# Performance work log

Measured on AMD Instinct MI355X. Metric: run time of the kernel, lower is better.

The kernel has to match this reference:

```python
import jax, jax.numpy as jnp
import numpy as np

N_NODES = 100_000
N_EDGES = 1_600_000
N_GRAPHS = 512
D_NODE = 128
H = 128
L_EXTRA = 2  # model_layer - 1


def _bn(x, g, b, eps=1e-5):
    # BatchNorm1d, training-mode math (biased batch variance), eval dropout = identity
    mu = jnp.mean(x, axis=0)
    var = jnp.var(x, axis=0)
    return g * (x - mu) * jax.lax.rsqrt(var + eps) + b


def _gin_conv(x, src, dst, W1, b1, bng, bnb, W2, b2):
    # GINConv (eps=0): mlp(x + sum_{j->i} x_j); mlp = Lin -> BN -> ReLU -> Lin
    agg = jax.ops.segment_sum(x[src], dst, num_segments=x.shape[0])
    h = x + agg
    h = jax.nn.relu(_bn(h @ W1 + b1, bng, bnb))
    return h @ W2 + b2


def setup_inputs():
    key = jax.random.key(0)
    ks = jax.random.split(key, 24)
    s = 0.05
    d = {}
    d["x"] = jax.random.normal(ks[0], (N_NODES, D_NODE), dtype=jnp.float32)
    d["edge_index"] = jax.random.randint(ks[1], (2, N_EDGES), 0, N_NODES, dtype=jnp.int32)
    d["batch"] = jnp.sort(jax.random.randint(ks[2], (N_NODES,), 0, N_GRAPHS, dtype=jnp.int32))
    d["vn_emb"] = jax.random.normal(ks[3], (1, H)) * s
    # conv1 MLP: Linear(D_NODE, 2H) -> BN -> ReLU -> Linear(2H, H)
    d["c1_W1"] = jax.random.normal(ks[4], (D_NODE, 2 * H)) * s
    d["c1_b1"] = jnp.zeros((2 * H,))
    d["c1_bng"] = jnp.ones((2 * H,))
    d["c1_bnb"] = jnp.zeros((2 * H,))
    d["c1_W2"] = jax.random.normal(ks[5], (2 * H, H)) * s
    d["c1_b2"] = jnp.zeros((H,))
    d["bn1_g"] = jnp.ones((H,))
    d["bn1_b"] = jnp.zeros((H,))
    # stacked extra GIN layers (model_layer - 1)
    d["cW1"] = jax.random.normal(ks[6], (L_EXTRA, H, 2 * H)) * s
    d["cb1"] = jnp.zeros((L_EXTRA, 2 * H))
    d["cbng"] = jnp.ones((L_EXTRA, 2 * H))
    d["cbnb"] = jnp.zeros((L_EXTRA, 2 * H))
    d["cW2"] = jax.random.normal(ks[7], (L_EXTRA, 2 * H, H)) * s
    d["cb2"] = jnp.zeros((L_EXTRA, H))
    d["bns_g"] = jnp.ones((L_EXTRA, H))
    d["bns_b"] = jnp.zeros((L_EXTRA, H))
    # virtual node MLP: Lin(H,2H)->BN->ReLU->Lin(2H,H)->BN->ReLU->Dropout
    d["vW1"] = jax.random.normal(ks[8], (H, 2 * H)) * s
    d["vb1"] = jnp.zeros((2 * H,))
    d["vbn1_g"] = jnp.ones((2 * H,))
    d["vbn1_b"] = jnp.zeros((2 * H,))
    d["vW2"] = jax.random.normal(ks[9], (2 * H, H)) * s
    d["vb2"] = jnp.zeros((H,))
    d["vbn2_g"] = jnp.ones((H,))
    d["vbn2_b"] = jnp.zeros((H,))
    return d


def reference(x, edge_index, batch, vn_emb, c1_W1, c1_b1, c1_bng, c1_bnb, c1_W2, c1_b2,
              bn1_g, bn1_b, cW1, cb1, cbng, cbnb, cW2, cb2, bns_g, bns_b,
              vW1, vb1, vbn1_g, vbn1_b, vW2, vb2, vbn2_g, vbn2_b):
    src, dst = edge_index[0], edge_index[1]
    # virtual node feature per graph: Embedding(1, H) indexed with zeros
    vfeat = jnp.broadcast_to(vn_emb[0], (N_GRAPHS, H))
    # layer 1: dropout is identity in eval mode
    post = jax.nn.relu(_bn(_gin_conv(x, src, dst, c1_W1, c1_b1, c1_bng, c1_bnb, c1_W2, c1_b2), bn1_g, bn1_b))
    for i in range(L_EXTRA):
        post = post + vfeat[batch]                       # virtual-node broadcast
        post = _bn(_gin_conv(post, src, dst, cW1[i], cb1[i], cbng[i], cbnb[i], cW2[i], cb2[i]), bns_g[i], bns_b[i])
        if i < L_EXTRA - 1:
            post = jax.nn.relu(post)
            pooled = jax.ops.segment_sum(post, batch, num_segments=N_GRAPHS)  # GlobalAddPool
            z = pooled + vfeat
            z = jax.nn.relu(_bn(z @ vW1 + vb1, vbn1_g, vbn1_b))
            vfeat = jax.nn.relu(_bn(z @ vW2 + vb2, vbn2_g, vbn2_b))
    # readout: global mean pool over nodes per graph
    counts = jax.ops.segment_sum(jnp.ones((x.shape[0],), post.dtype), batch, num_segments=N_GRAPHS)
    out = jax.ops.segment_sum(post, batch, num_segments=N_GRAPHS) / jnp.maximum(counts, 1.0)[:, None]
    return out
```

## Files before the change

kernel.cpp:

```cpp
#include <hip/hip_runtime.h>

#define NN 100000
#define NE 1600000
#define NG 512
#define DH 128
#define DH2 256
#define SCB 98
#define NSTRIPE 32

typedef __attribute__((ext_vector_type(8))) _Float16 h8;
typedef __attribute__((ext_vector_type(2))) _Float16 h2;
typedef __attribute__((ext_vector_type(4))) float f4;

static inline size_t align256(size_t x) { return (x + 255) & ~size_t(255); }

__global__ __launch_bounds__(256) void countslot_k(const int* __restrict__ ei,
                                                   int* __restrict__ cursor,
                                                   int* __restrict__ slot) {
    int i = blockIdx.x * blockDim.x + threadIdx.x;
    int stride = gridDim.x * blockDim.x;
    for (int e = i; e < NE; e += stride)
        slot[e] = atomicAdd(&cursor[ei[NE + e]], 1);
}

__global__ __launch_bounds__(256) void place_k(const int* __restrict__ ei,
                                               const int* __restrict__ rowptr,
                                               const int* __restrict__ slot,
                                               int* __restrict__ esrc) {
    int i = blockIdx.x * blockDim.x + threadIdx.x;
    int stride = gridDim.x * blockDim.x;
    for (int e = i; e < NE; e += stride)
        esrc[rowptr[ei[NE + e]] + slot[e]] = ei[e];
}

__global__ void gbound_k(const int* __restrict__ batch, int* __restrict__ gcnt) {
    int g = blockIdx.x * blockDim.x + threadIdx.x;
    if (g >= NG) return;
    int lo = 0, hi = NN;
    while (lo < hi) { int m = (lo + hi) >> 1; if (batch[m] < g) lo = m + 1; else hi = m; }
    int b0 = lo;
    lo = 0; hi = NN;
    int g1 = g + 1;
    while (lo < hi) { int m = (lo + hi) >> 1; if (batch[m] < g1) lo = m + 1; else hi = m; }
    gcnt[g] = lo - b0;
}

__global__ __launch_bounds__(256) void scan1_k(const int* __restrict__ deg,
                                               int* __restrict__ part) {
    int i0 = blockIdx.x * 1024 + threadIdx.x * 4;
    int s = 0;
    if (i0 < NN) {
        int4 v = *(const int4*)(deg + i0);
        s = v.x + v.y + v.z + v.w;
    }
#pragma unroll
    for (int o = 1; o < 64; o <<= 1) s += __shfl_xor(s, o);
    __shared__ int ws[4];
    if ((threadIdx.x & 63) == 0) ws[threadIdx.x >> 6] = s;
    __syncthreads();
    if (threadIdx.x == 0) part[blockIdx.x] = ws[0] + ws[1] + ws[2] + ws[3];
}

__global__ void scan2_k(int* __restrict__ part, int* __restrict__ rowptr) {
    if (threadIdx.x == 0) {
        int run = 0;
        for (int i = 0; i < SCB; i++) { int v = part[i]; part[i] = run; run += v; }
        rowptr[NN] = run;
    }
}

__global__ __launch_bounds__(256) void scan3_k(const int* __restrict__ deg,
                                               const int* __restrict__ part,
                                               int* __restrict__ rowptr) {
    int t = threadIdx.x;
    int i0 = blockIdx.x * 1024 + t * 4;
    int4 v = {0, 0, 0, 0};
    if (i0 < NN) v = *(const int4*)(deg + i0);
    int s = v.x + v.y + v.z + v.w;
    __shared__ int sc[256];
    sc[t] = s;
    __syncthreads();
    for (int o = 1; o < 256; o <<= 1) {
        int add = (t >= o) ? sc[t - o] : 0;
        __syncthreads();
        sc[t] += add;
        __syncthreads();
    }
    int excl = (t ? sc[t - 1] : 0) + part[blockIdx.x];
    if (i0 < NN) {
        int4 r;
        r.x = excl;
        r.y = excl + v.x;
        r.z = excl + v.x + v.y;
        r.w = excl + v.x + v.y + v.z;
        *(int4*)(rowptr + i0) = r;
    }
}

__global__ void castx_k(const float* __restrict__ x, _Float16* __restrict__ xh) {
    int i = blockIdx.x * blockDim.x + threadIdx.x;
    if (i >= NN * 16) return;
    const float4* s = (const float4*)x + i * 2;
    float4 p = s[0], q = s[1];
    h8 h = {(_Float16)p.x, (_Float16)p.y, (_Float16)p.z, (_Float16)p.w,
            (_Float16)q.x, (_Float16)q.y, (_Float16)q.z, (_Float16)q.w};
    ((h8*)xh)[i] = h;
}

__global__ void vinit_k(const float* __restrict__ emb, _Float16* __restrict__ vfeat) {
    int i = blockIdx.x * blockDim.x + threadIdx.x;
    if (i < NG * DH) vfeat[i] = (_Float16)emb[i & (DH - 1)];
}

__global__ void zin_k(const float* __restrict__ pooled, const _Float16* __restrict__ vf,
                      _Float16* __restrict__ zb) {
    int i = blockIdx.x * blockDim.x + threadIdx.x;
    if (i < NG * DH) zb[i] = (_Float16)(pooled[i] + (float)vf[i]);
}

__global__ void addvn_k(_Float16* __restrict__ x, const _Float16* __restrict__ vfeat,
                        const int* __restrict__ batch) {
    int i = blockIdx.x * blockDim.x + threadIdx.x;
    if (i >= NN * 16) return;
    int row = i >> 4;
    int bg = batch[row];
    h8 u = ((h8*)x)[i];
    h8 v = ((const h8*)vfeat)[bg * 16 + (i & 15)];
    h8 o;
#pragma unroll
    for (int e = 0; e < 8; e++) o[e] = (_Float16)((float)u[e] + (float)v[e]);
    ((h8*)x)[i] = o;
}

__global__ void finalout_k(const float* __restrict__ pooled2, const int* __restrict__ gcnt,
                           float* __restrict__ outp) {
    int i = blockIdx.x * blockDim.x + threadIdx.x;
    if (i >= NG * DH) return;
    float cnt = (float)gcnt[i >> 7];
    outp[i] = pooled2[i] / fmaxf(cnt, 1.0f);
}

__global__ void bnfin_k(const float* __restrict__ csum, const float* __restrict__ csq,
                        const float* __restrict__ g, const float* __restrict__ b,
                        float* __restrict__ scale, float* __restrict__ shift,
                        int NC, int M) {
    int col = threadIdx.x;
    if (col >= NC) return;
    float s = 0.f, q = 0.f;
    for (int st = 0; st < NSTRIPE; st++) { s += csum[st * NC + col]; q += csq[st * NC + col]; }
    float invM = 1.0f / (float)M;
    float mean = s * invM;
    float var = q * invM - mean * mean;
    float sc = g[col] * rsqrtf(var + 1e-5f);
    scale[col] = sc;
    shift[col] = b[col] - mean * sc;
}

struct WPack {
    const float* w[8];
    _Float16* wt[8];
    int K[8];
    int N[8];
};
__global__ void wtrans_k(WPack p) {
    int id = blockIdx.z;
    const float* W = p.w[id];
    _Float16* Wt = p.wt[id];
    int K = p.K[id], N = p.N[id];
    int n0 = blockIdx.x * 32, k0 = blockIdx.y * 32;
    if (n0 >= N || k0 >= K) return;
    __shared__ float t[32][33];
    int tx = threadIdx.x & 31, ty = threadIdx.x >> 5;
    for (int i = 0; i < 32; i += 8)
        t[ty + i][tx] = W[(size_t)(k0 + ty + i) * N + n0 + tx];
    __syncthreads();
    for (int i = 0; i < 32; i += 8)
        Wt[(size_t)(n0 + ty + i) * K + k0 + tx] = (_Float16)t[tx][ty + i];
}

__global__ __launch_bounds__(256) void agg_k(const _Float16* __restrict__ xin,
                                             const int* __restrict__ rowptr,
                                             const int* __restrict__ esrc,
                                             _Float16* __restrict__ out) {
    int wave = threadIdx.x >> 6, lane = threadIdx.x & 63;
    int node = blockIdx.x * 4 + wave;
    if (node >= NN) return;
    const h2* xr = (const h2*)xin;
    h2 self = xr[(size_t)node * 64 + lane];
    float a0 = (float)self.x, a1 = (float)self.y;
    int beg = rowptr[node], end = rowptr[node + 1];
    int j = beg;
    for (; j + 7 < end; j += 8) {
        int s0 = esrc[j],     s1 = esrc[j + 1], s2 = esrc[j + 2], s3 = esrc[j + 3];
        int s4 = esrc[j + 4], s5 = esrc[j + 5], s6 = esrc[j + 6], s7 = esrc[j + 7];
        h2 u0 = xr[(size_t)s0 * 64 + lane];
        h2 u1 = xr[(size_t)s1 * 64 + lane];
        h2 u2 = xr[(size_t)s2 * 64 + lane];
        h2 u3 = xr[(size_t)s3 * 64 + lane];
        h2 u4 = xr[(size_t)s4 * 64 + lane];
        h2 u5 = xr[(size_t)s5 * 64 + lane];
        h2 u6 = xr[(size_t)s6 * 64 + lane];
        h2 u7 = xr[(size_t)s7 * 64 + lane];
        a0 += ((float)u0.x + (float)u1.x) + ((float)u2.x + (float)u3.x)
            + ((float)u4.x + (float)u5.x) + ((float)u6.x + (float)u7.x);
        a1 += ((float)u0.y + (float)u1.y) + ((float)u2.y + (float)u3.y)
            + ((float)u4.y + (float)u5.y) + ((float)u6.y + (float)u7.y);
    }
    for (; j < end; j++) {
        h2 u = xr[(size_t)esrc[j] * 64 + lane];
        a0 += (float)u.x; a1 += (float)u.y;
    }
    h2 o; o.x = (_Float16)a0; o.y = (_Float16)a1;
    ((h2*)out)[(size_t)node * 64 + lane] = o;
}

__global__ __launch_bounds__(256, 2) void gemmA_k(
        const _Float16* __restrict__ A, const _Float16* __restrict__ Wt,
        const float* __restrict__ bias, _Float16* __restrict__ C,
        float* __restrict__ csum, float* __restrict__ csq, int M) {
    constexpr int K = 128, NCF = 256;
    constexpr int LDA = K + 8;
    __shared__ __align__(16) _Float16 As[128 * LDA];
    const int tid = threadIdx.x;
    const int lane = tid & 63;
    const int wave = tid >> 6;
    const int wr = wave & 1, wc = wave >> 1;
    const int lm = lane & 15, lq = lane >> 4;
    const int mB = blockIdx.x * 128;

    const int sr = tid >> 4;
    const int sc = (tid & 15) * 8;
#pragma unroll
    for (int rr = 0; rr < 128; rr += 16) {
        int gr = mB + rr + sr; if (gr >= M) gr = M - 1;
        *(h8*)&As[(rr + sr) * LDA + sc] = *(const h8*)&A[(size_t)gr * K + sc];
    }
    __syncthreads();

    f4 acc[4][8];
#pragma unroll
    for (int i = 0; i < 4; i++)
#pragma unroll
        for (int jj = 0; jj < 8; jj++) acc[i][jj] = (f4){0.f, 0.f, 0.f, 0.f};
#pragma unroll
    for (int ct = 0; ct < 2; ct++) {
        const int n0 = ct * 128 + wc * 64;
#pragma unroll
        for (int ks = 0; ks < 4; ks++) {
            h8 af[4], bf[4];
#pragma unroll
            for (int t = 0; t < 4; t++) {
                af[t] = *(const h8*)&As[(wr * 64 + t * 16 + lm) * LDA + ks * 32 + lq * 8];
                bf[t] = *(const h8*)&Wt[(size_t)(n0 + t * 16 + lm) * K + ks * 32 + lq * 8];
            }
#pragma unroll
            for (int i = 0; i < 4; i++)
#pragma unroll
                for (int j = 0; j < 4; j++)
                    acc[i][ct * 4 + j] =
                        __builtin_amdgcn_mfma_f32_16x16x32_f16(af[i], bf[j], acc[i][ct * 4 + j], 0, 0, 0);
        }
    }

    float bv[8];
#pragma unroll
    for (int jj = 0; jj < 8; jj++) bv[jj] = bias[(jj >> 2) * 128 + wc * 64 + (jj & 3) * 16 + lm];
    float ls[8] = {0, 0, 0, 0, 0, 0, 0, 0}, lsq[8] = {0, 0, 0, 0, 0, 0, 0, 0};
    _Float16* Cs = As;
    const int trow = tid >> 4;
    const int tcol = (tid & 15) * 8;
#pragma unroll
    for (int half = 0; half < 2; half++) {
        __syncthreads();
#pragma unroll
        for (int i = 0; i < 4; i++) {
            int row = wr * 64 + i * 16 + lq * 4;
#pragma unroll
            for (int j = 0; j < 4; j++) {
                int jj = half * 4 + j;
#pragma unroll
                for (int r = 0; r < 4; r++) {
                    float v = acc[i][jj][r] + bv[jj];
                    Cs[(row + r) * LDA + wc * 64 + j * 16 + lm] = (_Float16)v;
                    if (mB + row + r < M) { ls[jj] += v; lsq[jj] += v * v; }
                }
            }
        }
        __syncthreads();
#pragma unroll
        for (int p = 0; p < 8; p++) {
            int row = p * 16 + trow;
            int grow = mB + row;
            if (grow < M) {
                h8 v = *(const h8*)&Cs[row * LDA + tcol];
                *(h8*)&C[(size_t)grow * NCF + half * 128 + tcol] = v;
            }
        }
    }
    const int stripe = blockIdx.x & (NSTRIPE - 1);
#pragma unroll
    for (int jj = 0; jj < 8; jj++) {
        float s = ls[jj], q = lsq[jj];
        s += __shfl_xor(s, 16); s += __shfl_xor(s, 32);
        q += __shfl_xor(q, 16); q += __shfl_xor(q, 32);
        if (lq == 0) {
            int col = (jj >> 2) * 128 + wc * 64 + (jj & 3) * 16 + lm;
            atomicAdd(&csum[stripe * NCF + col], s);
            atomicAdd(&csq[stripe * NCF + col], q);
        }
    }
}

__global__ __launch_bounds__(256, 2) void gemmB_k(
        const _Float16* __restrict__ A, const _Float16* __restrict__ Wt,
        const float* __restrict__ bias, _Float16* __restrict__ C,
        float* __restrict__ csum, float* __restrict__ csq, int M,
        const float* __restrict__ bnsc, const float* __restrict__ bnsh) {
    constexpr int K = 256, NCF = 128, BK = 128;
    constexpr int LDA = BK + 8;
    __shared__ __align__(16) _Float16 As[128 * LDA];
    const int tid = threadIdx.x;
    const int lane = tid & 63;
    const int wave = tid >> 6;
    const int wr = wave & 1, wc = wave >> 1;
    const int lm = lane & 15, lq = lane >> 4;
    const int mB = blockIdx.x * 128;
    const int n0 = wc * 64;

    f4 acc[4][4];
#pragma unroll
    for (int i = 0; i < 4; i++)
#pragma unroll
        for (int j = 0; j < 4; j++) acc[i][j] = (f4){0.f, 0.f, 0.f, 0.f};

    const int sr = tid >> 4;
    const int sc = (tid & 15) * 8;

    for (int kc = 0; kc < K; kc += BK) {
        if (kc) __syncthreads();
        float bscv[8], bshv[8];
        {
            float4 s0 = *(const float4*)&bnsc[kc + sc];
            float4 s1 = *(const float4*)&bnsc[kc + sc + 4];
            float4 t0 = *(const float4*)&bnsh[kc + sc];
            float4 t1 = *(const float4*)&bnsh[kc + sc + 4];
            bscv[0] = s0.x; bscv[1] = s0.y; bscv[2] = s0.z; bscv[3] = s0.w;
            bscv[4] = s1.x; bscv[5] = s1.y; bscv[6] = s1.z; bscv[7] = s1.w;
            bshv[0] = t0.x; bshv[1] = t0.y; bshv[2] = t0.z; bshv[3] = t0.w;
            bshv[4] = t1.x; bshv[5] = t1.y; bshv[6] = t1.z; bshv[7] = t1.w;
        }
#pragma unroll
        for (int rr = 0; rr < 128; rr += 16) {
            int gr = mB + rr + sr; if (gr >= M) gr = M - 1;
            h8 h = *(const h8*)&A[(size_t)gr * K + kc + sc];
#pragma unroll
            for (int e = 0; e < 8; e++)
                h[e] = (_Float16)fmaxf((float)h[e] * bscv[e] + bshv[e], 0.f);
            *(h8*)&As[(rr + sr) * LDA + sc] = h;
        }
        __syncthreads();
#pragma unroll
        for (int ks = 0; ks < BK / 32; ks++) {
            h8 af[4], bf[4];
#pragma unroll
            for (int t = 0; t < 4; t++) {
                af[t] = *(const h8*)&As[(wr * 64 + t * 16 + lm) * LDA + ks * 32 + lq * 8];
                bf[t] = *(const h8*)&Wt[(size_t)(n0 + t * 16 + lm) * K + kc + ks * 32 + lq * 8];
            }
#pragma unroll
            for (int i = 0; i < 4; i++)
#pragma unroll
                for (int j = 0; j < 4; j++)
                    acc[i][j] = __builtin_amdgcn_mfma_f32_16x16x32_f16(af[i], bf[j], acc[i][j], 0, 0, 0);
        }
    }

    float bv[4];
#pragma unroll
    for (int j = 0; j < 4; j++) bv[j] = bias[n0 + j * 16 + lm];
    float ls[4] = {0, 0, 0, 0}, lsq[4] = {0, 0, 0, 0};
    __syncthreads();
    _Float16* Cs = As;
#pragma unroll
    for (int i = 0; i < 4; i++) {
        int row = wr * 64 + i * 16 + lq * 4;
        bool rv[4];
#pragma unroll
        for (int r = 0; r < 4; r++) rv[r] = (mB + row + r) < M;
#pragma unroll
        for (int j = 0; j < 4; j++) {
#pragma unroll
            for (int r = 0; r < 4; r++) {
                float v = acc[i][j][r] + bv[j];
                Cs[(row + r) * LDA + wc * 64 + j * 16 + lm] = (_Float16)v;
                if (rv[r]) { ls[j] += v; lsq[j] += v * v; }
            }
        }
    }
    const int stripe = blockIdx.x & (NSTRIPE - 1);
#pragma unroll
    for (int j = 0; j < 4; j++) {
        float s = ls[j], q = lsq[j];
        s += __shfl_xor(s, 16); s += __shfl_xor(s, 32);
        q += __shfl_xor(q, 16); q += __shfl_xor(q, 32);
        if (lq == 0) {
            atomicAdd(&csum[stripe * NCF + n0 + j * 16 + lm], s);
            atomicAdd(&csq[stripe * NCF + n0 + j * 16 + lm], q);
        }
    }
    __syncthreads();
    const int trow = tid >> 4;
    const int tcol = (tid & 15) * 8;
#pragma unroll
    for (int p = 0; p < 8; p++) {
        int row = p * 16 + trow;
        int grow = mB + row;
        if (grow < M) {
            h8 v = *(const h8*)&Cs[row * LDA + tcol];
            *(h8*)&C[(size_t)grow * NCF + tcol] = v;
        }
    }
}

__global__ void bnrelu_k(const _Float16* __restrict__ in, _Float16* __restrict__ out,
                         const float* __restrict__ scale, const float* __restrict__ shift,
                         const _Float16* __restrict__ vfeat, const int* __restrict__ batch,
                         int M) {
    constexpr int PER = 16;
    int tid = blockIdx.x * blockDim.x + threadIdx.x;
    int c8 = tid % PER;
    int c0 = c8 * 8;
    float sc[8], sh[8];
    float4 s0 = *(const float4*)&scale[c0];
    float4 s1 = *(const float4*)&scale[c0 + 4];
    float4 t0 = *(const float4*)&shift[c0];
    float4 t1 = *(const float4*)&shift[c0 + 4];
    sc[0] = s0.x; sc[1] = s0.y; sc[2] = s0.z; sc[3] = s0.w;
    sc[4] = s1.x; sc[5] = s1.y; sc[6] = s1.z; sc[7] = s1.w;
    sh[0] = t0.x; sh[1] = t0.y; sh[2] = t0.z; sh[3] = t0.w;
    sh[4] = t1.x; sh[5] = t1.y; sh[6] = t1.z; sh[7] = t1.w;
    int total = M * PER;
    int stride = gridDim.x * blockDim.x;
    for (int i = tid; i < total; i += stride) {
        int row = i / PER;
        h8 u = ((const h8*)in)[i];
        h8 w;
        bool vn = (vfeat != nullptr);
        if (vn) w = ((const h8*)vfeat)[batch[row] * PER + c8];
        h8 o;
#pragma unroll
        for (int e = 0; e < 8; e++) {
            float vv = fmaxf((float)u[e] * sc[e] + sh[e], 0.f);
            if (vn) vv += (float)w[e];
            o[e] = (_Float16)vv;
        }
        ((h8*)out)[i] = o;
    }
}

__global__ __launch_bounds__(256) void bnpool_k(
        const _Float16* __restrict__ in, _Float16* __restrict__ out,
        const float* __restrict__ scale, const float* __restrict__ shift,
        const int* __restrict__ batch, float* __restrict__ pooled,
        int M, int relu) {
    int t = threadIdx.x;
    int c0 = (t & 63) * 2;
    int r0 = blockIdx.x * 128 + (t >> 6) * 32;
    float sc0 = scale[c0], h0 = shift[c0];
    float sc1 = scale[c0 + 1], h1 = shift[c0 + 1];
    int rend = r0 + 32; if (rend > M) rend = M;
    float a0 = 0.f, a1 = 0.f; int cur = -1;
    int r = r0;
    for (; r + 1 < rend; r += 2) {
        h2 ua = ((const h2*)in)[(size_t)r * 64 + (c0 >> 1)];
        h2 ub = ((const h2*)in)[(size_t)(r + 1) * 64 + (c0 >> 1)];
        int bga = batch[r], bgb = batch[r + 1];
        float va0 = (float)ua.x * sc0 + h0, va1 = (float)ua.y * sc1 + h1;
        float vb0 = (float)ub.x * sc0 + h0, vb1 = (float)ub.y * sc1 + h1;
        if (relu) {
            va0 = fmaxf(va0, 0.f); va1 = fmaxf(va1, 0.f);
            vb0 = fmaxf(vb0, 0.f); vb1 = fmaxf(vb1, 0.f);
        }
        if (out) {
            h2 oa; oa.x = (_Float16)va0; oa.y = (_Float16)va1;
            h2 ob; ob.x = (_Float16)vb0; ob.y = (_Float16)vb1;
            ((h2*)out)[(size_t)r * 64 + (c0 >> 1)] = oa;
            ((h2*)out)[(size_t)(r + 1) * 64 + (c0 >> 1)] = ob;
        }
        if (bga != cur) {
            if (cur >= 0) {
                atomicAdd(&pooled[(size_t)cur * DH + c0], a0);
                atomicAdd(&pooled[(size_t)cur * DH + c0 + 1], a1);
            }
            cur = bga; a0 = 0.f; a1 = 0.f;
        }
        a0 += va0; a1 += va1;
        if (bgb != cur) {
            atomicAdd(&pooled[(size_t)cur * DH + c0], a0);
            atomicAdd(&pooled[(size_t)cur * DH + c0 + 1], a1);
            cur = bgb; a0 = 0.f; a1 = 0.f;
        }
        a0 += vb0; a1 += vb1;
    }
    for (; r < rend; r++) {
        h2 u = ((const h2*)in)[(size_t)r * 64 + (c0 >> 1)];
        float v0 = (float)u.x * sc0 + h0;
        float v1 = (float)u.y * sc1 + h1;
        if (relu) { v0 = fmaxf(v0, 0.f); v1 = fmaxf(v1, 0.f); }
        if (out) { h2 o; o.x = (_Float16)v0; o.y = (_Float16)v1; ((h2*)out)[(size_t)r * 64 + (c0 >> 1)] = o; }
        int bg = batch[r];
        if (bg != cur) {
            if (cur >= 0) {
                atomicAdd(&pooled[(size_t)cur * DH + c0], a0);
                atomicAdd(&pooled[(size_t)cur * DH + c0 + 1], a1);
            }
            cur = bg; a0 = 0.f; a1 = 0.f;
        }
        a0 += v0; a1 += v1;
    }
    if (cur >= 0) {
        atomicAdd(&pooled[(size_t)cur * DH + c0], a0);
        atomicAdd(&pooled[(size_t)cur * DH + c0 + 1], a1);
    }
}

extern "C" void kernel_launch(void* const* d_in, const int* in_sizes, int n_in,
                              void* d_out, int out_size, void* d_ws, size_t ws_size,
                              hipStream_t stream) {
    const float* x      = (const float*)d_in[0];
    const int*   ei     = (const int*)d_in[1];
    const int*   batch  = (const int*)d_in[2];
    const float* vn_emb = (const float*)d_in[3];
    const float* c1_W1  = (const float*)d_in[4];
    const float* c1_b1  = (const float*)d_in[5];
    const float* c1_bng = (const float*)d_in[6];
    const float* c1_bnb = (const float*)d_in[7];
    const float* c1_W2  = (const float*)d_in[8];
    const float* c1_b2  = (const float*)d_in[9];
    const float* bn1_g  = (const float*)d_in[10];
    const float* bn1_b  = (const float*)d_in[11];
    const float* cW1    = (const float*)d_in[12];
    const float* cb1    = (const float*)d_in[13];
    const float* cbng   = (const float*)d_in[14];
    const float* cbnb   = (const float*)d_in[15];
    const float* cW2    = (const float*)d_in[16];
    const float* cb2    = (const float*)d_in[17];
    const float* bns_g  = (const float*)d_in[18];
    const float* bns_b  = (const float*)d_in[19];
    const float* vW1    = (const float*)d_in[20];
    const float* vb1    = (const float*)d_in[21];
    const float* vbn1_g = (const float*)d_in[22];
    const float* vbn1_b = (const float*)d_in[23];
    const float* vW2    = (const float*)d_in[24];
    const float* vb2    = (const float*)d_in[25];
    const float* vbn2_g = (const float*)d_in[26];
    const float* vbn2_b = (const float*)d_in[27];
    float* outp = (float*)d_out;
    (void)in_sizes; (void)n_in; (void)out_size; (void)ws_size;

    char* w = (char*)d_ws;
    size_t off = 0;
    auto carve = [&](size_t bytes) -> void* {
        void* p = w + off; off = align256(off + bytes); return p;
    };
    int*   cursor  = (int*)carve((size_t)NN * 4);
    float* pooled  = (float*)carve((size_t)NG * DH * 4);
    float* pooled2 = (float*)carve((size_t)NG * DH * 4);
    float *sA[3], *qA[3], *sB[3], *qB[3], *sV1, *qV1, *sV2, *qV2;
    for (int i = 0; i < 3; i++) {
        sA[i] = (float*)carve((size_t)NSTRIPE * 256 * 4);
        qA[i] = (float*)carve((size_t)NSTRIPE * 256 * 4);
    }
    for (int i = 0; i < 3; i++) {
        sB[i] = (float*)carve((size_t)NSTRIPE * 128 * 4);
        qB[i] = (float*)carve((size_t)NSTRIPE * 128 * 4);
    }
    sV1 = (float*)carve((size_t)NSTRIPE * 256 * 4);
    qV1 = (float*)carve((size_t)NSTRIPE * 256 * 4);
    sV2 = (float*)carve((size_t)NSTRIPE * 128 * 4);
    qV2 = (float*)carve((size_t)NSTRIPE * 128 * 4);
    size_t zbytes = off;
    float *scA[3], *shA[3], *scB[3], *shB[3];
    for (int i = 0; i < 3; i++) { scA[i] = (float*)carve(256 * 4); shA[i] = (float*)carve(256 * 4); }
    for (int i = 0; i < 3; i++) { scB[i] = (float*)carve(128 * 4); shB[i] = (float*)carve(128 * 4); }
    float* scV1 = (float*)carve(256 * 4); float* shV1 = (float*)carve(256 * 4);
    float* scV2 = (float*)carve(128 * 4); float* shV2 = (float*)carve(128 * 4);
    int*   gcnt    = (int*)carve((size_t)NG * 4);
    int*   rowptr  = (int*)carve((size_t)(NN + 1) * 4);
    int*   slot    = (int*)carve((size_t)NE * 4);
    int*   esrc    = (int*)carve((size_t)NE * 4);
    int*   part    = (int*)carve((size_t)SCB * 4);
    _Float16* vfeat = (_Float16*)carve((size_t)NG * DH * 2);
    _Float16* zin   = (_Float16*)carve((size_t)NG * DH * 2);
    _Float16* zb    = (_Float16*)carve((size_t)NG * DH2 * 2);
    _Float16* vraw  = (_Float16*)carve((size_t)NG * DH * 2);
    _Float16* xh    = (_Float16*)carve((size_t)NN * DH * 2);
    _Float16* hb    = (_Float16*)carve((size_t)NN * DH * 2);
    _Float16* b1    = (_Float16*)carve((size_t)NN * DH2 * 2);
    _Float16* abuf  = (_Float16*)carve((size_t)NN * DH * 2);
    _Float16* Wt[8];
    for (int i = 0; i < 8; i++) Wt[i] = (_Float16*)carve((size_t)DH * DH2 * 2);

    WPack wp;
    wp.w[0] = c1_W1;            wp.K[0] = 128; wp.N[0] = 256;
    wp.w[1] = c1_W2;            wp.K[1] = 256; wp.N[1] = 128;
    wp.w[2] = cW1;              wp.K[2] = 128; wp.N[2] = 256;
    wp.w[3] = cW2;              wp.K[3] = 256; wp.N[3] = 128;
    wp.w[4] = cW1 + 128 * 256;  wp.K[4] = 128; wp.N[4] = 256;
    wp.w[5] = cW2 + 256 * 128;  wp.K[5] = 256; wp.N[5] = 128;
    wp.w[6] = vW1;              wp.K[6] = 128; wp.N[6] = 256;
    wp.w[7] = vW2;              wp.K[7] = 256; wp.N[7] = 128;
    for (int i = 0; i < 8; i++) wp.wt[i] = Wt[i];

    const int GB = (NN + 127) / 128;

    hipMemsetAsync(d_ws, 0, zbytes, stream);
    countslot_k<<<782, 256, 0, stream>>>(ei, cursor, slot);
    scan1_k<<<SCB, 256, 0, stream>>>(cursor, part);
    scan2_k<<<1, 64, 0, stream>>>(part, rowptr);
    scan3_k<<<SCB, 256, 0, stream>>>(cursor, part, rowptr);
    place_k<<<782, 256, 0, stream>>>(ei, rowptr, slot, esrc);
    gbound_k<<<2, 256, 0, stream>>>(batch, gcnt);
    wtrans_k<<<dim3(8, 8, 8), 256, 0, stream>>>(wp);
    vinit_k<<<(NG * DH + 255) / 256, 256, 0, stream>>>(vn_emb, vfeat);
    castx_k<<<(NN * 16 + 255) / 256, 256, 0, stream>>>(x, xh);

    agg_k<<<NN / 4, 256, 0, stream>>>(xh, rowptr, esrc, hb);
    gemmA_k<<<GB, 256, 0, stream>>>(hb, Wt[0], c1_b1, b1, sA[0], qA[0], NN);
    bnfin_k<<<1, 256, 0, stream>>>(sA[0], qA[0], c1_bng, c1_bnb, scA[0], shA[0], 256, NN);
    gemmB_k<<<GB, 256, 0, stream>>>(b1, Wt[1], c1_b2, abuf, sB[0], qB[0], NN, scA[0], shA[0]);
    bnfin_k<<<1, 256, 0, stream>>>(sB[0], qB[0], bn1_g, bn1_b, scB[0], shB[0], 128, NN);
    bnrelu_k<<<2048, 256, 0, stream>>>(abuf, abuf, scB[0], shB[0], vfeat, batch, NN);

    agg_k<<<NN / 4, 256, 0, stream>>>(abuf, rowptr, esrc, hb);
    gemmA_k<<<GB, 256, 0, stream>>>(hb, Wt[2], cb1, b1, sA[1], qA[1], NN);
    bnfin_k<<<1, 256, 0, stream>>>(sA[1], qA[1], cbng, cbnb, scA[1], shA[1], 256, NN);
    gemmB_k<<<GB, 256, 0, stream>>>(b1, Wt[3], cb2, abuf, sB[1], qB[1], NN, scA[1], shA[1]);
    bnfin_k<<<1, 256, 0, stream>>>(sB[1], qB[1], bns_g, bns_b, scB[1], shB[1], 128, NN);
    bnpool_k<<<GB, 256, 0, stream>>>(abuf, abuf, scB[1], shB[1], batch, pooled, NN, 1);

    zin_k<<<(NG * DH + 255) / 256, 256, 0, stream>>>(pooled, vfeat, zin);
    gemmA_k<<<4, 256, 0, stream>>>(zin, Wt[6], vb1, zb, sV1, qV1, NG);
    bnfin_k<<<1, 256, 0, stream>>>(sV1, qV1, vbn1_g, vbn1_b, scV1, shV1, 256, NG);
    gemmB_k<<<4, 256, 0, stream>>>(zb, Wt[7], vb2, vraw, sV2, qV2, NG, scV1, shV1);
    bnfin_k<<<1, 256, 0, stream>>>(sV2, qV2, vbn2_g, vbn2_b, scV2, shV2, 128, NG);
    bnrelu_k<<<32, 256, 0, stream>>>(vraw, vfeat, scV2, shV2, nullptr, nullptr, NG);

    addvn_k<<<(NN * 16 + 255) / 256, 256, 0, stream>>>(abuf, vfeat, batch);
    agg_k<<<NN / 4, 256, 0, stream>>>(abuf, rowptr, esrc, hb);
    gemmA_k<<<GB, 256, 0, stream>>>(hb, Wt[4], cb1 + 256, b1, sA[2], qA[2], NN);
    bnfin_k<<<1, 256, 0, stream>>>(sA[2], qA[2], cbng + 256, cbnb + 256, scA[2], shA[2], 256, NN);
    gemmB_k<<<GB, 256, 0, stream>>>(b1, Wt[5], cb2 + 128, abuf, sB[2], qB[2], NN, scA[2], shA[2]);
    bnfin_k<<<1, 256, 0, stream>>>(sB[2], qB[2], bns_g + 128, bns_b + 128, scB[2], shB[2], 128, NN);
    bnpool_k<<<GB, 256, 0, stream>>>(abuf, nullptr, scB[2], shB[2], batch, pooled2, NN, 0);

    finalout_k<<<(NG * DH + 255) / 256, 256, 0, stream>>>(pooled2, gcnt, outp);
}
```

Baseline: 810.3 us.

## Fuse neighbor aggregation into first GEMM and fold virtual-node add into gather

```diff
diff --git a/kernel.cpp b/kernel.cpp
--- a/kernel.cpp
+++ b/kernel.cpp
@@ -62,11 +62,20 @@
 }
 
 __global__ void scan2_k(int* __restrict__ part, int* __restrict__ rowptr) {
-    if (threadIdx.x == 0) {
-        int run = 0;
-        for (int i = 0; i < SCB; i++) { int v = part[i]; part[i] = run; run += v; }
-        rowptr[NN] = run;
-    }
+    int t = threadIdx.x;
+    int v = (t < SCB) ? part[t] : 0;
+    int s = v;
+#pragma unroll
+    for (int o = 1; o < 64; o <<= 1) {
+        int u = __shfl_up(s, o);
+        if ((t & 63) >= o) s += u;
+    }
+    __shared__ int wtot[2];
+    if ((t & 63) == 63) wtot[t >> 6] = s;
+    __syncthreads();
+    if (t >= 64) s += wtot[0];
+    if (t < SCB) part[t] = s - v;
+    if (t == SCB - 1) rowptr[NN] = s;
 }
 
 __global__ __launch_bounds__(256) void scan3_k(const int* __restrict__ deg,
@@ -116,20 +125,6 @@
                       _Float16* __restrict__ zb) {
     int i = blockIdx.x * blockDim.x + threadIdx.x;
     if (i < NG * DH) zb[i] = (_Float16)(pooled[i] + (float)vf[i]);
-}
-
-__global__ void addvn_k(_Float16* __restrict__ x, const _Float16* __restrict__ vfeat,
-                        const int* __restrict__ batch) {
-    int i = blockIdx.x * blockDim.x + threadIdx.x;
-    if (i >= NN * 16) return;
-    int row = i >> 4;
-    int bg = batch[row];
-    h8 u = ((h8*)x)[i];
-    h8 v = ((const h8*)vfeat)[bg * 16 + (i & 15)];
-    h8 o;
-#pragma unroll
-    for (int e = 0; e < 8; e++) o[e] = (_Float16)((float)u[e] + (float)v[e]);
-    ((h8*)x)[i] = o;
 }
 
 __global__ void finalout_k(const float* __restrict__ pooled2, const int* __restrict__ gcnt,
@@ -178,40 +173,160 @@
         Wt[(size_t)(n0 + ty + i) * K + k0 + tx] = (_Float16)t[tx][ty + i];
 }
 
-__global__ __launch_bounds__(256) void agg_k(const _Float16* __restrict__ xin,
-                                             const int* __restrict__ rowptr,
-                                             const int* __restrict__ esrc,
-                                             _Float16* __restrict__ out) {
-    int wave = threadIdx.x >> 6, lane = threadIdx.x & 63;
-    int node = blockIdx.x * 4 + wave;
-    if (node >= NN) return;
-    const h2* xr = (const h2*)xin;
-    h2 self = xr[(size_t)node * 64 + lane];
-    float a0 = (float)self.x, a1 = (float)self.y;
-    int beg = rowptr[node], end = rowptr[node + 1];
-    int j = beg;
-    for (; j + 7 < end; j += 8) {
-        int s0 = esrc[j],     s1 = esrc[j + 1], s2 = esrc[j + 2], s3 = esrc[j + 3];
-        int s4 = esrc[j + 4], s5 = esrc[j + 5], s6 = esrc[j + 6], s7 = esrc[j + 7];
-        h2 u0 = xr[(size_t)s0 * 64 + lane];
-        h2 u1 = xr[(size_t)s1 * 64 + lane];
-        h2 u2 = xr[(size_t)s2 * 64 + lane];
-        h2 u3 = xr[(size_t)s3 * 64 + lane];
-        h2 u4 = xr[(size_t)s4 * 64 + lane];
-        h2 u5 = xr[(size_t)s5 * 64 + lane];
-        h2 u6 = xr[(size_t)s6 * 64 + lane];
-        h2 u7 = xr[(size_t)s7 * 64 + lane];
-        a0 += ((float)u0.x + (float)u1.x) + ((float)u2.x + (float)u3.x)
-            + ((float)u4.x + (float)u5.x) + ((float)u6.x + (float)u7.x);
-        a1 += ((float)u0.y + (float)u1.y) + ((float)u2.y + (float)u3.y)
-            + ((float)u4.y + (float)u5.y) + ((float)u6.y + (float)u7.y);
-    }
-    for (; j < end; j++) {
-        h2 u = xr[(size_t)esrc[j] * 64 + lane];
-        a0 += (float)u.x; a1 += (float)u.y;
-    }
-    h2 o; o.x = (_Float16)a0; o.y = (_Float16)a1;
-    ((h2*)out)[(size_t)node * 64 + lane] = o;
+__global__ __launch_bounds__(256, 2) void aggemmA_k(
+        const _Float16* __restrict__ X,
+        const int* __restrict__ rowptr, const int* __restrict__ esrc,
+        const _Float16* __restrict__ vfeat, const int* __restrict__ batch,
+        const _Float16* __restrict__ Wt,
+        const float* __restrict__ bias, _Float16* __restrict__ C,
+        float* __restrict__ csum, float* __restrict__ csq, int M) {
+    constexpr int K = 128, NCF = 256;
+    constexpr int LDA = K + 8;
+    __shared__ __align__(16) _Float16 As[128 * LDA];
+    const int tid = threadIdx.x;
+    const int lane = tid & 63;
+    const int wave = tid >> 6;
+    const int wr = wave & 1, wc = wave >> 1;
+    const int lm = lane & 15, lq = lane >> 4;
+    const int mB = blockIdx.x * 128;
+
+    const h2* xr = (const h2*)X;
+    const h2* vr = (const h2*)vfeat;
+    for (int rr = 0; rr < 32; rr++) {
+        int row = wave * 32 + rr;
+        int gr = mB + row; if (gr >= M) gr = M - 1;
+        h2 self = xr[(size_t)gr * 64 + lane];
+        float a0 = (float)self.x, a1 = (float)self.y;
+        int beg = rowptr[gr], end = rowptr[gr + 1];
+        int j = beg;
+        if (vfeat == nullptr) {
+            for (; j + 7 < end; j += 8) {
+                int s0 = esrc[j],     s1 = esrc[j + 1], s2 = esrc[j + 2], s3 = esrc[j + 3];
+                int s4 = esrc[j + 4], s5 = esrc[j + 5], s6 = esrc[j + 6], s7 = esrc[j + 7];
+                h2 u0 = xr[(size_t)s0 * 64 + lane];
+                h2 u1 = xr[(size_t)s1 * 64 + lane];
+                h2 u2 = xr[(size_t)s2 * 64 + lane];
+                h2 u3 = xr[(size_t)s3 * 64 + lane];
+                h2 u4 = xr[(size_t)s4 * 64 + lane];
+                h2 u5 = xr[(size_t)s5 * 64 + lane];
+                h2 u6 = xr[(size_t)s6 * 64 + lane];
+                h2 u7 = xr[(size_t)s7 * 64 + lane];
+                a0 += ((float)u0.x + (float)u1.x) + ((float)u2.x + (float)u3.x)
+                    + ((float)u4.x + (float)u5.x) + ((float)u6.x + (float)u7.x);
+                a1 += ((float)u0.y + (float)u1.y) + ((float)u2.y + (float)u3.y)
+                    + ((float)u4.y + (float)u5.y) + ((float)u6.y + (float)u7.y);
+            }
+            for (; j < end; j++) {
+                h2 u = xr[(size_t)esrc[j] * 64 + lane];
+                a0 += (float)u.x; a1 += (float)u.y;
+            }
+        } else {
+            {
+                h2 v = vr[(size_t)batch[gr] * 64 + lane];
+                a0 += (float)v.x; a1 += (float)v.y;
+            }
+            for (; j + 3 < end; j += 4) {
+                int s0 = esrc[j], s1 = esrc[j + 1], s2 = esrc[j + 2], s3 = esrc[j + 3];
+                int g0 = batch[s0], g1 = batch[s1], g2 = batch[s2], g3 = batch[s3];
+                h2 u0 = xr[(size_t)s0 * 64 + lane];
+                h2 u1 = xr[(size_t)s1 * 64 + lane];
+                h2 u2 = xr[(size_t)s2 * 64 + lane];
+                h2 u3 = xr[(size_t)s3 * 64 + lane];
+                h2 v0 = vr[(size_t)g0 * 64 + lane];
+                h2 v1 = vr[(size_t)g1 * 64 + lane];
+                h2 v2 = vr[(size_t)g2 * 64 + lane];
+                h2 v3 = vr[(size_t)g3 * 64 + lane];
+                a0 += ((float)u0.x + (float)v0.x) + ((float)u1.x + (float)v1.x)
+                    + ((float)u2.x + (float)v2.x) + ((float)u3.x + (float)v3.x);
+                a1 += ((float)u0.y + (float)v0.y) + ((float)u1.y + (float)v1.y)
+                    + ((float)u2.y + (float)v2.y) + ((float)u3.y + (float)v3.y);
+            }
+            for (; j < end; j++) {
+                int s0 = esrc[j];
+                int g0 = batch[s0];
+                h2 u = xr[(size_t)s0 * 64 + lane];
+                h2 v = vr[(size_t)g0 * 64 + lane];
+                a0 += (float)u.x + (float)v.x;
+                a1 += (float)u.y + (float)v.y;
+            }
+        }
+        h2 o; o.x = (_Float16)a0; o.y = (_Float16)a1;
+        *(h2*)&As[row * LDA + lane * 2] = o;
+    }
+    __syncthreads();
+
+    f4 acc[4][8];
+#pragma unroll
+    for (int i = 0; i < 4; i++)
+#pragma unroll
+        for (int jj = 0; jj < 8; jj++) acc[i][jj] = (f4){0.f, 0.f, 0.f, 0.f};
+#pragma unroll
+    for (int ct = 0; ct < 2; ct++) {
+        const int n0 = ct * 128 + wc * 64;
+#pragma unroll
+        for (int ks = 0; ks < 4; ks++) {
+            h8 af[4], bf[4];
+#pragma unroll
+            for (int t = 0; t < 4; t++) {
+                af[t] = *(const h8*)&As[(wr * 64 + t * 16 + lm) * LDA + ks * 32 + lq * 8];
+                bf[t] = *(const h8*)&Wt[(size_t)(n0 + t * 16 + lm) * K + ks * 32 + lq * 8];
+            }
+#pragma unroll
+            for (int i = 0; i < 4; i++)
+#pragma unroll
+                for (int j = 0; j < 4; j++)
+                    acc[i][ct * 4 + j] =
+                        __builtin_amdgcn_mfma_f32_16x16x32_f16(af[i], bf[j], acc[i][ct * 4 + j], 0, 0, 0);
+        }
+    }
+
+    float bv[8];
+#pragma unroll
+    for (int jj = 0; jj < 8; jj++) bv[jj] = bias[(jj >> 2) * 128 + wc * 64 + (jj & 3) * 16 + lm];
+    float ls[8] = {0, 0, 0, 0, 0, 0, 0, 0}, lsq[8] = {0, 0, 0, 0, 0, 0, 0, 0};
+    _Float16* Cs = As;
+    const int trow = tid >> 4;
+    const int tcol = (tid & 15) * 8;
+#pragma unroll
+    for (int half = 0; half < 2; half++) {
+        __syncthreads();
+#pragma unroll
+        for (int i = 0; i < 4; i++) {
+            int row = wr * 64 + i * 16 + lq * 4;
+#pragma unroll
+            for (int j = 0; j < 4; j++) {
+                int jj = half * 4 + j;
+#pragma unroll
+                for (int r = 0; r < 4; r++) {
+                    float v = acc[i][jj][r] + bv[jj];
+                    Cs[(row + r) * LDA + wc * 64 + j * 16 + lm] = (_Float16)v;
+                    if (mB + row + r < M) { ls[jj] += v; lsq[jj] += v * v; }
+                }
+            }
+        }
+        __syncthreads();
+#pragma unroll
+        for (int p = 0; p < 8; p++) {
+            int row = p * 16 + trow;
+            int grow = mB + row;
+            if (grow < M) {
+                h8 v = *(const h8*)&Cs[row * LDA + tcol];
+                *(h8*)&C[(size_t)grow * NCF + half * 128 + tcol] = v;
+            }
+        }
+    }
+    const int stripe = blockIdx.x & (NSTRIPE - 1);
+#pragma unroll
+    for (int jj = 0; jj < 8; jj++) {
+        float s = ls[jj], q = lsq[jj];
+        s += __shfl_xor(s, 16); s += __shfl_xor(s, 32);
+        q += __shfl_xor(q, 16); q += __shfl_xor(q, 32);
+        if (lq == 0) {
+            int col = (jj >> 2) * 128 + wc * 64 + (jj & 3) * 16 + lm;
+            atomicAdd(&csum[stripe * NCF + col], s);
+            atomicAdd(&csq[stripe * NCF + col], q);
+        }
+    }
 }
 
 __global__ __launch_bounds__(256, 2) void gemmA_k(
@@ -595,7 +710,6 @@
     _Float16* zb    = (_Float16*)carve((size_t)NG * DH2 * 2);
     _Float16* vraw  = (_Float16*)carve((size_t)NG * DH * 2);
     _Float16* xh    = (_Float16*)carve((size_t)NN * DH * 2);
-    _Float16* hb    = (_Float16*)carve((size_t)NN * DH * 2);
     _Float16* b1    = (_Float16*)carve((size_t)NN * DH2 * 2);
     _Float16* abuf  = (_Float16*)carve((size_t)NN * DH * 2);
     _Float16* Wt[8];
@@ -617,7 +731,7 @@
     hipMemsetAsync(d_ws, 0, zbytes, stream);
     countslot_k<<<782, 256, 0, stream>>>(ei, cursor, slot);
     scan1_k<<<SCB, 256, 0, stream>>>(cursor, part);
-    scan2_k<<<1, 64, 0, stream>>>(part, rowptr);
+    scan2_k<<<1, 128, 0, stream>>>(part, rowptr);
     scan3_k<<<SCB, 256, 0, stream>>>(cursor, part, rowptr);
     place_k<<<782, 256, 0, stream>>>(ei, rowptr, slot, esrc);
     gbound_k<<<2, 256, 0, stream>>>(batch, gcnt);
@@ -625,15 +739,15 @@
     vinit_k<<<(NG * DH + 255) / 256, 256, 0, stream>>>(vn_emb, vfeat);
     castx_k<<<(NN * 16 + 255) / 256, 256, 0, stream>>>(x, xh);
 
-    agg_k<<<NN / 4, 256, 0, stream>>>(xh, rowptr, esrc, hb);
-    gemmA_k<<<GB, 256, 0, stream>>>(hb, Wt[0], c1_b1, b1, sA[0], qA[0], NN);
+    aggemmA_k<<<GB, 256, 0, stream>>>(xh, rowptr, esrc, nullptr, nullptr,
+                                      Wt[0], c1_b1, b1, sA[0], qA[0], NN);
     bnfin_k<<<1, 256, 0, stream>>>(sA[0], qA[0], c1_bng, c1_bnb, scA[0], shA[0], 256, NN);
     gemmB_k<<<GB, 256, 0, stream>>>(b1, Wt[1], c1_b2, abuf, sB[0], qB[0], NN, scA[0], shA[0]);
     bnfin_k<<<1, 256, 0, stream>>>(sB[0], qB[0], bn1_g, bn1_b, scB[0], shB[0], 128, NN);
     bnrelu_k<<<2048, 256, 0, stream>>>(abuf, abuf, scB[0], shB[0], vfeat, batch, NN);
 
-    agg_k<<<NN / 4, 256, 0, stream>>>(abuf, rowptr, esrc, hb);
-    gemmA_k<<<GB, 256, 0, stream>>>(hb, Wt[2], cb1, b1, sA[1], qA[1], NN);
+    aggemmA_k<<<GB, 256, 0, stream>>>(abuf, rowptr, esrc, nullptr, nullptr,
+                                      Wt[2], cb1, b1, sA[1], qA[1], NN);
     bnfin_k<<<1, 256, 0, stream>>>(sA[1], qA[1], cbng, cbnb, scA[1], shA[1], 256, NN);
     gemmB_k<<<GB, 256, 0, stream>>>(b1, Wt[3], cb2, abuf, sB[1], qB[1], NN, scA[1], shA[1]);
     bnfin_k<<<1, 256, 0, stream>>>(sB[1], qB[1], bns_g, bns_b, scB[1], shB[1], 128, NN);
@@ -646,9 +760,8 @@
     bnfin_k<<<1, 256, 0, stream>>>(sV2, qV2, vbn2_g, vbn2_b, scV2, shV2, 128, NG);
     bnrelu_k<<<32, 256, 0, stream>>>(vraw, vfeat, scV2, shV2, nullptr, nullptr, NG);
 
-    addvn_k<<<(NN * 16 + 255) / 256, 256, 0, stream>>>(abuf, vfeat, batch);
-    agg_k<<<NN / 4, 256, 0, stream>>>(abuf, rowptr, esrc, hb);
-    gemmA_k<<<GB, 256, 0, stream>>>(hb, Wt[4], cb1 + 256, b1, sA[2], qA[2], NN);
+    aggemmA_k<<<GB, 256, 0, stream>>>(abuf, rowptr, esrc, vfeat, batch,
+                                      Wt[4], cb1 + 256, b1, sA[2], qA[2], NN);
     bnfin_k<<<1, 256, 0, stream>>>(sA[2], qA[2], cbng + 256, cbnb + 256, scA[2], shA[2], 256, NN);
     gemmB_k<<<GB, 256, 0, stream>>>(b1, Wt[5], cb2 + 128, abuf, sB[2], qB[2], NN, scA[2], shA[2]);
     bnfin_k<<<1, 256, 0, stream>>>(sB[2], qB[2], bns_g + 128, bns_b + 128, scB[2], shB[2], 128, NN);
```

After: 1.311 ms. +61.7%, slower.

## Widen aggregation gathers to 16-byte rows and fuse virtual-node add

Applied to the files above, without the earlier changes.

```diff
diff --git a/kernel.cpp b/kernel.cpp
--- a/kernel.cpp
+++ b/kernel.cpp
@@ -62,11 +62,20 @@
 }
 
 __global__ void scan2_k(int* __restrict__ part, int* __restrict__ rowptr) {
-    if (threadIdx.x == 0) {
-        int run = 0;
-        for (int i = 0; i < SCB; i++) { int v = part[i]; part[i] = run; run += v; }
-        rowptr[NN] = run;
-    }
+    int t = threadIdx.x;
+    int v = (t < SCB) ? part[t] : 0;
+    int s = v;
+#pragma unroll
+    for (int o = 1; o < 64; o <<= 1) {
+        int u = __shfl_up(s, o);
+        if ((t & 63) >= o) s += u;
+    }
+    __shared__ int wtot[2];
+    if ((t & 63) == 63) wtot[t >> 6] = s;
+    __syncthreads();
+    if (t >= 64) s += wtot[0];
+    if (t < SCB) part[t] = s - v;
+    if (t == SCB - 1) rowptr[NN] = s;
 }
 
 __global__ __launch_bounds__(256) void scan3_k(const int* __restrict__ deg,
@@ -116,20 +125,6 @@
                       _Float16* __restrict__ zb) {
     int i = blockIdx.x * blockDim.x + threadIdx.x;
     if (i < NG * DH) zb[i] = (_Float16)(pooled[i] + (float)vf[i]);
-}
-
-__global__ void addvn_k(_Float16* __restrict__ x, const _Float16* __restrict__ vfeat,
-                        const int* __restrict__ batch) {
-    int i = blockIdx.x * blockDim.x + threadIdx.x;
-    if (i >= NN * 16) return;
-    int row = i >> 4;
-    int bg = batch[row];
-    h8 u = ((h8*)x)[i];
-    h8 v = ((const h8*)vfeat)[bg * 16 + (i & 15)];
-    h8 o;
-#pragma unroll
-    for (int e = 0; e < 8; e++) o[e] = (_Float16)((float)u[e] + (float)v[e]);
-    ((h8*)x)[i] = o;
 }
 
 __global__ void finalout_k(const float* __restrict__ pooled2, const int* __restrict__ gcnt,
@@ -181,37 +176,84 @@
 __global__ __launch_bounds__(256) void agg_k(const _Float16* __restrict__ xin,
                                              const int* __restrict__ rowptr,
                                              const int* __restrict__ esrc,
+                                             const _Float16* __restrict__ vfeat,
+                                             const int* __restrict__ batch,
                                              _Float16* __restrict__ out) {
     int wave = threadIdx.x >> 6, lane = threadIdx.x & 63;
     int node = blockIdx.x * 4 + wave;
     if (node >= NN) return;
-    const h2* xr = (const h2*)xin;
-    h2 self = xr[(size_t)node * 64 + lane];
-    float a0 = (float)self.x, a1 = (float)self.y;
+    const int sub = lane >> 4, li = lane & 15;
+    const h8* xr = (const h8*)xin;
+    const h8* vr = (const h8*)vfeat;
+    float a[8] = {0.f, 0.f, 0.f, 0.f, 0.f, 0.f, 0.f, 0.f};
+    if (sub == 0) {
+        h8 s = xr[(size_t)node * 16 + li];
+#pragma unroll
+        for (int e = 0; e < 8; e++) a[e] = (float)s[e];
+        if (vfeat) {
+            h8 v = vr[(size_t)batch[node] * 16 + li];
+#pragma unroll
+            for (int e = 0; e < 8; e++) a[e] += (float)v[e];
+        }
+    }
     int beg = rowptr[node], end = rowptr[node + 1];
     int j = beg;
-    for (; j + 7 < end; j += 8) {
-        int s0 = esrc[j],     s1 = esrc[j + 1], s2 = esrc[j + 2], s3 = esrc[j + 3];
-        int s4 = esrc[j + 4], s5 = esrc[j + 5], s6 = esrc[j + 6], s7 = esrc[j + 7];
-        h2 u0 = xr[(size_t)s0 * 64 + lane];
-        h2 u1 = xr[(size_t)s1 * 64 + lane];
-        h2 u2 = xr[(size_t)s2 * 64 + lane];
-        h2 u3 = xr[(size_t)s3 * 64 + lane];
-        h2 u4 = xr[(size_t)s4 * 64 + lane];
-        h2 u5 = xr[(size_t)s5 * 64 + lane];
-        h2 u6 = xr[(size_t)s6 * 64 + lane];
-        h2 u7 = xr[(size_t)s7 * 64 + lane];
-        a0 += ((float)u0.x + (float)u1.x) + ((float)u2.x + (float)u3.x)
-            + ((float)u4.x + (float)u5.x) + ((float)u6.x + (float)u7.x);
-        a1 += ((float)u0.y + (float)u1.y) + ((float)u2.y + (float)u3.y)
-            + ((float)u4.y + (float)u5.y) + ((float)u6.y + (float)u7.y);
-    }
-    for (; j < end; j++) {
-        h2 u = xr[(size_t)esrc[j] * 64 + lane];
-        a0 += (float)u.x; a1 += (float)u.y;
-    }
-    h2 o; o.x = (_Float16)a0; o.y = (_Float16)a1;
-    ((h2*)out)[(size_t)node * 64 + lane] = o;
+    if (vfeat == nullptr) {
+        for (; j + 15 < end; j += 16) {
+            int e0 = esrc[j + sub], e1 = esrc[j + 4 + sub];
+            int e2 = esrc[j + 8 + sub], e3 = esrc[j + 12 + sub];
+            h8 u0 = xr[(size_t)e0 * 16 + li];
+            h8 u1 = xr[(size_t)e1 * 16 + li];
+            h8 u2 = xr[(size_t)e2 * 16 + li];
+            h8 u3 = xr[(size_t)e3 * 16 + li];
+#pragma unroll
+            for (int e = 0; e < 8; e++)
+                a[e] += ((float)u0[e] + (float)u1[e]) + ((float)u2[e] + (float)u3[e]);
+        }
+        for (; j < end; j += 4) {
+            int e = j + sub;
+            if (e < end) {
+                int s = esrc[e];
+                h8 u = xr[(size_t)s * 16 + li];
+#pragma unroll
+                for (int k = 0; k < 8; k++) a[k] += (float)u[k];
+            }
+        }
+    } else {
+        for (; j + 7 < end; j += 8) {
+            int e0 = esrc[j + sub], e1 = esrc[j + 4 + sub];
+            int g0 = batch[e0], g1 = batch[e1];
+            h8 u0 = xr[(size_t)e0 * 16 + li];
+            h8 u1 = xr[(size_t)e1 * 16 + li];
+            h8 v0 = vr[(size_t)g0 * 16 + li];
+            h8 v1 = vr[(size_t)g1 * 16 + li];
+#pragma unroll
+            for (int e = 0; e < 8; e++)
+                a[e] += ((float)u0[e] + (float)v0[e]) + ((float)u1[e] + (float)v1[e]);
+        }
+        for (; j < end; j += 4) {
+            int e = j + sub;
+            if (e < end) {
+                int s = esrc[e];
+                int g = batch[s];
+                h8 u = xr[(size_t)s * 16 + li];
+                h8 v = vr[(size_t)g * 16 + li];
+#pragma unroll
+                for (int k = 0; k < 8; k++) a[k] += (float)u[k] + (float)v[k];
+            }
+        }
+    }
+#pragma unroll
+    for (int e = 0; e < 8; e++) {
+        a[e] += __shfl_xor(a[e], 16);
+        a[e] += __shfl_xor(a[e], 32);
+    }
+    if (sub == 0) {
+        h8 o;
+#pragma unroll
+        for (int e = 0; e < 8; e++) o[e] = (_Float16)a[e];
+        ((h8*)out)[(size_t)node * 16 + li] = o;
+    }
 }
 
 __global__ __launch_bounds__(256, 2) void gemmA_k(
@@ -617,7 +659,7 @@
     hipMemsetAsync(d_ws, 0, zbytes, stream);
     countslot_k<<<782, 256, 0, stream>>>(ei, cursor, slot);
     scan1_k<<<SCB, 256, 0, stream>>>(cursor, part);
-    scan2_k<<<1, 64, 0, stream>>>(part, rowptr);
+    scan2_k<<<1, 128, 0, stream>>>(part, rowptr);
     scan3_k<<<SCB, 256, 0, stream>>>(cursor, part, rowptr);
     place_k<<<782, 256, 0, stream>>>(ei, rowptr, slot, esrc);
     gbound_k<<<2, 256, 0, stream>>>(batch, gcnt);
@@ -625,14 +667,14 @@
     vinit_k<<<(NG * DH + 255) / 256, 256, 0, stream>>>(vn_emb, vfeat);
     castx_k<<<(NN * 16 + 255) / 256, 256, 0, stream>>>(x, xh);
 
-    agg_k<<<NN / 4, 256, 0, stream>>>(xh, rowptr, esrc, hb);
+    agg_k<<<NN / 4, 256, 0, stream>>>(xh, rowptr, esrc, nullptr, nullptr, hb);
     gemmA_k<<<GB, 256, 0, stream>>>(hb, Wt[0], c1_b1, b1, sA[0], qA[0], NN);
     bnfin_k<<<1, 256, 0, stream>>>(sA[0], qA[0], c1_bng, c1_bnb, scA[0], shA[0], 256, NN);
     gemmB_k<<<GB, 256, 0, stream>>>(b1, Wt[1], c1_b2, abuf, sB[0], qB[0], NN, scA[0], shA[0]);
     bnfin_k<<<1, 256, 0, stream>>>(sB[0], qB[0], bn1_g, bn1_b, scB[0], shB[0], 128, NN);
     bnrelu_k<<<2048, 256, 0, stream>>>(abuf, abuf, scB[0], shB[0], vfeat, batch, NN);
 
-    agg_k<<<NN / 4, 256, 0, stream>>>(abuf, rowptr, esrc, hb);
+    agg_k<<<NN / 4, 256, 0, stream>>>(abuf, rowptr, esrc, nullptr, nullptr, hb);
     gemmA_k<<<GB, 256, 0, stream>>>(hb, Wt[2], cb1, b1, sA[1], qA[1], NN);
     bnfin_k<<<1, 256, 0, stream>>>(sA[1], qA[1], cbng, cbnb, scA[1], shA[1], 256, NN);
     gemmB_k<<<GB, 256, 0, stream>>>(b1, Wt[3], cb2, abuf, sB[1], qB[1], NN, scA[1], shA[1]);
@@ -646,8 +688,7 @@
     bnfin_k<<<1, 256, 0, stream>>>(sV2, qV2, vbn2_g, vbn2_b, scV2, shV2, 128, NG);
     bnrelu_k<<<32, 256, 0, stream>>>(vraw, vfeat, scV2, shV2, nullptr, nullptr, NG);
 
-    addvn_k<<<(NN * 16 + 255) / 256, 256, 0, stream>>>(abuf, vfeat, batch);
-    agg_k<<<NN / 4, 256, 0, stream>>>(abuf, rowptr, esrc, hb);
+    agg_k<<<NN / 4, 256, 0, stream>>>(abuf, rowptr, esrc, vfeat, batch, hb);
     gemmA_k<<<GB, 256, 0, stream>>>(hb, Wt[4], cb1 + 256, b1, sA[2], qA[2], NN);
     bnfin_k<<<1, 256, 0, stream>>>(sA[2], qA[2], cbng + 256, cbnb + 256, scA[2], shA[2], 256, NN);
     gemmB_k<<<GB, 256, 0, stream>>>(b1, Wt[5], cb2 + 128, abuf, sB[2], qB[2], NN, scA[2], shA[2]);
```

Measured after the change: 787.4 us. 1.03x faster.
